# Optimization experiments

Measured on AMD Instinct MI355X. Metric: run time of the kernel, lower is better.

The kernel has to match this reference:

```python
import jax, jax.numpy as jnp
import numpy as np

N_NODES = 100000
N_EDGES = 1000000
D_IN = 64
D_OUT = 64


def setup_inputs() -> dict:
    key = jax.random.key(0)
    k_x, k_e, k_w, k_b = jax.random.split(key, 4)
    x = jax.random.normal(k_x, (N_NODES, D_IN), dtype=jnp.float32)
    edge_index = jax.random.randint(k_e, (2, N_EDGES), 0, N_NODES, dtype=jnp.int64)
    # degrees of destination nodes (what the caller is expected to supply);
    # clamp to >=1 to avoid division by zero for isolated nodes
    deg = jax.ops.segment_sum(jnp.ones((N_EDGES,), jnp.float32), edge_index[1], num_segments=N_NODES)
    node_degrees = jnp.maximum(deg, 1.0)
    W = jax.random.normal(k_w, (D_OUT, D_IN), dtype=jnp.float32) * (1.0 / np.sqrt(D_IN))
    b = jax.random.normal(k_b, (D_OUT,), dtype=jnp.float32) * 0.01
    return {"x": x, "edge_index": edge_index, "node_degrees": node_degrees, "W": W, "b": b}


def reference(x, edge_index, node_degrees, W, b):
    # Original does argsort+cumsum+boundary segment-sum; mathematically this is
    # a scatter-add of gathered neighbor features into dst, i.e. a segment sum.
    src, dst = edge_index[0], edge_index[1]
    agg = jax.ops.segment_sum(x[src], dst, num_segments=x.shape[0])  # [N, D_IN]
    mean = agg / node_degrees[:, None]
    return mean @ W.T + b  # [N, D_OUT]
```

## Files before the change

### kernel.cpp

```cpp
#include <hip/hip_runtime.h>


#define D 64
#define BSHIFT 7
#define BNODES (1 << BSHIFT)
#define CAP 2048
#define GTHREADS 512
#define PERTHREAD (CAP / GTHREADS)
#define PXW_THREADS 512
#define MAXB 2048

__device__ inline int detect_stride_block(const unsigned* __restrict__ words,
                                          int E, int* sflag) {
    int t = threadIdx.x;
    if (t < 64) {
        unsigned v = (t < E) ? words[2 * t + 1] : 0u;
        int any = __any(v != 0u);
        if (t == 0) *sflag = any ? 1 : 2;
    }
    __syncthreads();
    return *sflag;
}

__device__ inline unsigned pack_bf16(float a, float b) {
    unsigned ua = __float_as_uint(a), ub = __float_as_uint(b);
    ua += 0x7fffu + ((ua >> 16) & 1u);
    ub += 0x7fffu + ((ub >> 16) & 1u);
    return (ua >> 16) | (ub & 0xffff0000u);
}

__global__ __launch_bounds__(PXW_THREADS, 4) void partition_xw_kernel(
        const unsigned* __restrict__ ewords, int* __restrict__ cursor,
        unsigned* __restrict__ pairs, uint2* __restrict__ spill,
        int* __restrict__ spillCnt,
        const float* __restrict__ x, const float* __restrict__ W,
        unsigned* __restrict__ y2, int E, int N, int nb, int pblocks) {
    __shared__ __align__(16) char smem[52240];
    int t = threadIdx.x;

    if ((int)blockIdx.x < pblocks) {
        int* lhist = (int*)smem;
        int* lbase = lhist + MAXB;
        int* sflag = lbase + MAXB;
        int s = detect_stride_block(ewords, E, sflag);
        int base = blockIdx.x * 8192;
        for (int i = t; i < nb; i += PXW_THREADS) lhist[i] = 0;
        __syncthreads();
        unsigned pv[16]; int bk[16];
        #pragma unroll
        for (int k = 0; k < 16; ++k) {
            int e = base + k * PXW_THREADS + t;
            bk[k] = -1;
            if (e < E) {
                unsigned src = ewords[(size_t)e * s];
                unsigned dst = ewords[((size_t)E + e) * s];
                bk[k] = (int)(dst >> BSHIFT);
                pv[k] = src | ((dst & (BNODES - 1)) << 17);
                atomicAdd(&lhist[bk[k]], 1);
            }
        }
        __syncthreads();
        for (int hb = t; hb < nb; hb += PXW_THREADS) {
            int cc = lhist[hb];
            if (cc) lbase[hb] = atomicAdd(&cursor[hb], cc);
            lhist[hb] = 0;
        }
        __syncthreads();
        #pragma unroll
        for (int k = 0; k < 16; ++k) {
            if (bk[k] >= 0) {
                int lpos = lbase[bk[k]] + atomicAdd(&lhist[bk[k]], 1);
                if (lpos < CAP) {
                    pairs[(size_t)bk[k] * CAP + lpos] = pv[k];
                } else {
                    int si = atomicAdd(spillCnt, 1);
                    unsigned dst = ((unsigned)bk[k] << BSHIFT) | (pv[k] >> 17);
                    spill[si] = make_uint2(pv[k] & 0x1FFFFu, dst);
                }
            }
        }
    } else {
        float* Wt = (float*)smem;
        float* xs = Wt + 64 * 68;
        for (int i = t; i < 64 * 64; i += PXW_THREADS) {
            int o = i >> 6, k = i & 63;
            Wt[k * 68 + o] = W[i];
        }
        int base = ((int)blockIdx.x - pblocks) * 128;
        int row = t >> 4, c4 = (t & 15) * 4;
        #pragma unroll
        for (int r = 0; r < 4; ++r) {
            int nl = row + r * 32;
            int n = base + nl;
            float4 v = {0.f, 0.f, 0.f, 0.f};
            if (n < N) v = *(const float4*)(x + (size_t)n * 64 + c4);
            *(float4*)&xs[nl * 68 + c4] = v;
        }
        __syncthreads();
        int o4 = (t & 15) * 4, nl4 = (t >> 4) * 4;
        float acc[4][4];
        #pragma unroll
        for (int i = 0; i < 4; ++i)
            #pragma unroll
            for (int j = 0; j < 4; ++j) acc[i][j] = 0.f;
        #pragma unroll 2
        for (int k0 = 0; k0 < 64; k0 += 4) {
            float a[4][4], wv[4][4];
            #pragma unroll
            for (int i = 0; i < 4; ++i)
                *(float4*)a[i] = *(const float4*)&xs[(nl4 + i) * 68 + k0];
            #pragma unroll
            for (int dk = 0; dk < 4; ++dk)
                *(float4*)wv[dk] = *(const float4*)&Wt[(k0 + dk) * 68 + o4];
            #pragma unroll
            for (int i = 0; i < 4; ++i)
                #pragma unroll
                for (int j = 0; j < 4; ++j)
                    acc[i][j] += a[i][0] * wv[0][j] + a[i][1] * wv[1][j]
                               + a[i][2] * wv[2][j] + a[i][3] * wv[3][j];
        }
        int n0 = base + nl4;
        #pragma unroll
        for (int i = 0; i < 4; ++i) {
            if (n0 + i < N) {
                uint2 p;
                p.x = pack_bf16(acc[i][0], acc[i][1]);
                p.y = pack_bf16(acc[i][2], acc[i][3]);
                *(uint2*)(y2 + (size_t)(n0 + i) * 32 + (o4 >> 1)) = p;
            }
        }
    }
}

__global__ __launch_bounds__(GTHREADS) void bucket_gather(
        const unsigned* __restrict__ y2, const unsigned* __restrict__ pairs,
        const int* __restrict__ cursor, const uint2* __restrict__ spill,
        const int* __restrict__ spillCnt,
        const float* __restrict__ deg, const float* __restrict__ b,
        float* __restrict__ out, int N) {
    __shared__ unsigned list[CAP];
    __shared__ int cnt[BNODES], st[BNODES], sc[BNODES];
    int t = threadIdx.x;
    int bkt = blockIdx.x, base = bkt << BSHIFT;
    int total = cursor[bkt];
    int cn = total < CAP ? total : CAP;
    int lane = t & 63, w = t >> 6;
    int g = lane >> 4, c = lane & 15;
    float4 bv = ((const float4*)b)[c];

    if (t < BNODES) cnt[t] = 0;
    __syncthreads();
    unsigned pv[PERTHREAD];
    #pragma unroll
    for (int j = 0; j < PERTHREAD; ++j) {
        int i = t + j * GTHREADS;
        pv[j] = (i < cn) ? pairs[(size_t)bkt * CAP + i] : 0xFFFFFFFFu;
        if (i < cn) atomicAdd(&cnt[pv[j] >> 17], 1);
    }
    __syncthreads();
    if (t < BNODES) sc[t] = cnt[t];
    __syncthreads();
    for (int off = 1; off < BNODES; off <<= 1) {
        int v = (t < BNODES && t >= off) ? sc[t - off] : 0;
        __syncthreads();
        if (t < BNODES) sc[t] += v;
        __syncthreads();
    }
    if (t < BNODES) { st[t] = sc[t] - cnt[t]; sc[t] = sc[t] - cnt[t]; }
    __syncthreads();
    #pragma unroll
    for (int j = 0; j < PERTHREAD; ++j) {
        if (pv[j] != 0xFFFFFFFFu) {
            int pos = atomicAdd(&sc[pv[j] >> 17], 1);
            list[pos] = pv[j] & 0x1FFFFu;
        }
    }
    __syncthreads();

    int scnt = *spillCnt;

    for (int nl0 = w * 16; nl0 < w * 16 + 16; nl0 += 4) {
        int mynode = nl0 + g;
        int n = base + mynode;
        int s0 = st[mynode], e1 = s0 + cnt[mynode];
        float ax = 0.f, ay = 0.f, az = 0.f, aw = 0.f;
        float bx = 0.f, by = 0.f, bz = 0.f, bw = 0.f;
        int i = s0;
        for (; i + 1 < e1; i += 2) {
            unsigned s0v = list[i], s1v = list[i + 1];
            uint2 u0 = *(const uint2*)(y2 + (size_t)s0v * 32 + c * 2);
            uint2 u1 = *(const uint2*)(y2 + (size_t)s1v * 32 + c * 2);
            ax += __uint_as_float(u0.x << 16);
            ay += __uint_as_float(u0.x & 0xffff0000u);
            az += __uint_as_float(u0.y << 16);
            aw += __uint_as_float(u0.y & 0xffff0000u);
            bx += __uint_as_float(u1.x << 16);
            by += __uint_as_float(u1.x & 0xffff0000u);
            bz += __uint_as_float(u1.y << 16);
            bw += __uint_as_float(u1.y & 0xffff0000u);
        }
        if (i < e1) {
            unsigned sv = list[i];
            uint2 u = *(const uint2*)(y2 + (size_t)sv * 32 + c * 2);
            ax += __uint_as_float(u.x << 16);
            ay += __uint_as_float(u.x & 0xffff0000u);
            az += __uint_as_float(u.y << 16);
            aw += __uint_as_float(u.y & 0xffff0000u);
        }
        ax += bx; ay += by; az += bz; aw += bw;
        for (int k = 0; k < scnt; ++k) {
            uint2 e = spill[k];
            if ((int)e.y == n) {
                uint2 u = *(const uint2*)(y2 + (size_t)e.x * 32 + c * 2);
                ax += __uint_as_float(u.x << 16);
                ay += __uint_as_float(u.x & 0xffff0000u);
                az += __uint_as_float(u.y << 16);
                aw += __uint_as_float(u.y & 0xffff0000u);
            }
        }
        if (n < N) {
            float invd = 1.0f / deg[n];
            float4 o4 = {ax * invd + bv.x, ay * invd + bv.y,
                         az * invd + bv.z, aw * invd + bv.w};
            *(float4*)(out + (size_t)n * 64 + c * 4) = o4;
        }
    }
}

__global__ __launch_bounds__(256) void scatter_kernel(
        const float* __restrict__ x, const unsigned* __restrict__ ewords,
        float* __restrict__ agg, int E) {
    __shared__ int sflag;
    int s = detect_stride_block(ewords, E, &sflag);
    int gid = blockIdx.x * blockDim.x + threadIdx.x;
    int e = gid >> 4, q = gid & 15;
    if (e >= E) return;
    int src = (int)ewords[(size_t)e * s];
    int dst = (int)ewords[((size_t)E + e) * s];
    const float4 v = *(const float4*)(x + (size_t)src * D + q * 4);
    float* p = agg + (size_t)dst * D + q * 4;
    unsafeAtomicAdd(p + 0, v.x);
    unsafeAtomicAdd(p + 1, v.y);
    unsafeAtomicAdd(p + 2, v.z);
    unsafeAtomicAdd(p + 3, v.w);
}

__global__ __launch_bounds__(256) void gemm_kernel(
        float* __restrict__ inout, const float* __restrict__ deg,
        const float* __restrict__ W, const float* __restrict__ b, int nNodes) {
    __shared__ float Wt[64 * 65];
    __shared__ float rows[4 * 64];
    int t = threadIdx.x;
    for (int i = t; i < 64 * 64; i += 256) {
        int o = i >> 6, k = i & 63;
        Wt[k * 65 + o] = W[i];
    }
    int base = blockIdx.x * 4;
    int nl = t >> 6, o = t & 63;
    int n = base + nl;
    if (n < nNodes) {
        float invd = 1.0f / deg[n];
        rows[nl * 64 + o] = inout[(size_t)n * 64 + o] * invd;
    }
    __syncthreads();
    if (n >= nNodes) return;
    float acc = b[o];
    #pragma unroll
    for (int k = 0; k < 64; ++k)
        acc += rows[nl * 64 + k] * Wt[k * 65 + o];
    inout[(size_t)n * 64 + o] = acc;
}

extern "C" void kernel_launch(void* const* d_in, const int* in_sizes, int n_in,
                              void* d_out, int out_size, void* d_ws, size_t ws_size,
                              hipStream_t stream) {
    const float*    x      = (const float*)d_in[0];
    const unsigned* ewords = (const unsigned*)d_in[1];
    const float*    deg    = (const float*)d_in[2];
    const float*    W      = (const float*)d_in[3];
    const float*    b      = (const float*)d_in[4];
    float*          out    = (float*)d_out;

    const int E = in_sizes[1] / 2;
    const int N = in_sizes[2];
    const int nb = (N + BNODES - 1) >> BSHIFT;

    char* ws = (char*)d_ws;
    size_t curB  = (MAXB + 16) * 4;
    size_t pairB = ((size_t)nb * CAP * 4 + 63) & ~63ull;
    size_t spB   = ((size_t)E * 8 + 63) & ~63ull;
    size_t need  = curB + pairB + spB + (size_t)N * 32 * 4;

    if (ws_size >= need && N < (1 << 17) && nb <= MAXB) {
        int*      cursor   = (int*)ws;
        int*      spillCnt = cursor + MAXB;
        unsigned* pairs    = (unsigned*)(ws + curB);
        uint2*    spill    = (uint2*)(ws + curB + pairB);
        unsigned* y2       = (unsigned*)(ws + curB + pairB + spB);

        hipMemsetAsync(cursor, 0, curB, stream);

        int pblocks  = (E + 8191) / 8192;
        int xwblocks = (N + 127) / 128;
        partition_xw_kernel<<<pblocks + xwblocks, PXW_THREADS, 0, stream>>>(
            ewords, cursor, pairs, spill, spillCnt, x, W, y2, E, N, nb, pblocks);

        bucket_gather<<<nb, GTHREADS, 0, stream>>>(
            y2, pairs, cursor, spill, spillCnt, deg, b, out, N);
    } else {
        hipMemsetAsync(d_out, 0, (size_t)out_size * sizeof(float), stream);
        long long sthreads = (long long)E * 16;
        int sblocks = (int)((sthreads + 255) / 256);
        scatter_kernel<<<sblocks, 256, 0, stream>>>(x, ewords, out, E);
        gemm_kernel<<<(N + 3) / 4, 256, 0, stream>>>(out, deg, W, b, N);
    }
}
```

Baseline: 140.8 us.

## Fuse memset, partition/XW and bucket gather into one cooperative persistent kernel

Replaces the memset plus two kernel launches with a single cooperative kernel on a fixed grid of 512 blocks. Phases are separated by grid-wide syncs, and blocks loop over virtual partition, XW and bucket work items. The XW tile shrinks from 128 to 64 nodes per block. This is meant to remove launch gaps and inter-kernel overhead, at the cost of grid-sync latency and possible load imbalance from the fixed grid. If the cooperative launch fails, it falls back to the original path.

```diff
diff --git a/kernel.cpp b/kernel.cpp
--- a/kernel.cpp
+++ b/kernel.cpp
@@ -1,4 +1,7 @@
 #include <hip/hip_runtime.h>
+#include <hip/hip_cooperative_groups.h>
+
+namespace cg = cooperative_groups;
 
 
 #define D 64
@@ -9,6 +12,7 @@
 #define PERTHREAD (CAP / GTHREADS)
 #define PXW_THREADS 512
 #define MAXB 2048
+#define COOP_GRID 512
 
 __device__ inline int detect_stride_block(const unsigned* __restrict__ words,
                                           int E, int* sflag) {
@@ -27,6 +31,210 @@
     ua += 0x7fffu + ((ua >> 16) & 1u);
     ub += 0x7fffu + ((ub >> 16) & 1u);
     return (ua >> 16) | (ub & 0xffff0000u);
+}
+
+__global__ __launch_bounds__(512, 4) void fused_all(
+        const unsigned* __restrict__ ewords, int* __restrict__ cursor,
+        unsigned* __restrict__ pairs, uint2* __restrict__ spill,
+        int* __restrict__ spillCnt,
+        const float* __restrict__ x, const float* __restrict__ W,
+        unsigned* __restrict__ y2,
+        const float* __restrict__ deg, const float* __restrict__ bias,
+        float* __restrict__ out,
+        int E, int N, int nb, int pblocks, int xwblocks) {
+    __shared__ __align__(16) char smem[34832];
+    int t = threadIdx.x;
+    cg::grid_group grid = cg::this_grid();
+
+    for (int i = blockIdx.x * 512 + t; i < MAXB + 16; i += gridDim.x * 512)
+        cursor[i] = 0;
+    grid.sync();
+
+    for (int vb = blockIdx.x; vb < pblocks + xwblocks; vb += gridDim.x) {
+        __syncthreads();
+        if (vb < pblocks) {
+            int* lhist = (int*)smem;
+            int* lbase = lhist + MAXB;
+            int* sflag = lbase + MAXB;
+            int s = detect_stride_block(ewords, E, sflag);
+            int base = vb * 8192;
+            for (int i = t; i < nb; i += 512) lhist[i] = 0;
+            __syncthreads();
+            unsigned pv[16]; int bk[16];
+            #pragma unroll
+            for (int k = 0; k < 16; ++k) {
+                int e = base + k * 512 + t;
+                bk[k] = -1;
+                if (e < E) {
+                    unsigned src = ewords[(size_t)e * s];
+                    unsigned dst = ewords[((size_t)E + e) * s];
+                    bk[k] = (int)(dst >> BSHIFT);
+                    pv[k] = src | ((dst & (BNODES - 1)) << 17);
+                    atomicAdd(&lhist[bk[k]], 1);
+                }
+            }
+            __syncthreads();
+            for (int hb = t; hb < nb; hb += 512) {
+                int cc = lhist[hb];
+                if (cc) lbase[hb] = atomicAdd(&cursor[hb], cc);
+                lhist[hb] = 0;
+            }
+            __syncthreads();
+            #pragma unroll
+            for (int k = 0; k < 16; ++k) {
+                if (bk[k] >= 0) {
+                    int lpos = lbase[bk[k]] + atomicAdd(&lhist[bk[k]], 1);
+                    if (lpos < CAP) {
+                        pairs[(size_t)bk[k] * CAP + lpos] = pv[k];
+                    } else {
+                        int si = atomicAdd(spillCnt, 1);
+                        unsigned dst = ((unsigned)bk[k] << BSHIFT) | (pv[k] >> 17);
+                        spill[si] = make_uint2(pv[k] & 0x1FFFFu, dst);
+                    }
+                }
+            }
+        } else {
+            float* Wt = (float*)smem;
+            float* xs = Wt + 64 * 68;
+            for (int i = t; i < 64 * 64; i += 512) {
+                int o = i >> 6, k = i & 63;
+                Wt[k * 68 + o] = W[i];
+            }
+            int base = (vb - pblocks) * 64;
+            int idx = t;
+            #pragma unroll
+            for (int r = 0; r < 2; ++r, idx += 512) {
+                int nl = idx >> 4, c4 = (idx & 15) * 4;
+                int n = base + nl;
+                float4 v = {0.f, 0.f, 0.f, 0.f};
+                if (n < N) v = *(const float4*)(x + (size_t)n * 64 + c4);
+                *(float4*)&xs[nl * 68 + c4] = v;
+            }
+            __syncthreads();
+            int o4 = (t & 15) * 4, nl2 = (t >> 4) * 2;
+            float acc[2][4];
+            #pragma unroll
+            for (int i = 0; i < 2; ++i)
+                #pragma unroll
+                for (int j = 0; j < 4; ++j) acc[i][j] = 0.f;
+            #pragma unroll 2
+            for (int k0 = 0; k0 < 64; k0 += 4) {
+                float a[2][4], wv[4][4];
+                #pragma unroll
+                for (int i = 0; i < 2; ++i)
+                    *(float4*)a[i] = *(const float4*)&xs[(nl2 + i) * 68 + k0];
+                #pragma unroll
+                for (int dk = 0; dk < 4; ++dk)
+                    *(float4*)wv[dk] = *(const float4*)&Wt[(k0 + dk) * 68 + o4];
+                #pragma unroll
+                for (int i = 0; i < 2; ++i)
+                    #pragma unroll
+                    for (int j = 0; j < 4; ++j)
+                        acc[i][j] += a[i][0] * wv[0][j] + a[i][1] * wv[1][j]
+                                   + a[i][2] * wv[2][j] + a[i][3] * wv[3][j];
+            }
+            int n0 = base + nl2;
+            #pragma unroll
+            for (int i = 0; i < 2; ++i) {
+                if (n0 + i < N) {
+                    uint2 p;
+                    p.x = pack_bf16(acc[i][0], acc[i][1]);
+                    p.y = pack_bf16(acc[i][2], acc[i][3]);
+                    *(uint2*)(y2 + (size_t)(n0 + i) * 32 + (o4 >> 1)) = p;
+                }
+            }
+        }
+    }
+    grid.sync();
+
+    int lane = t & 63, w = t >> 6;
+    int g = lane >> 4, c = lane & 15;
+    float4 bv = ((const float4*)bias)[c];
+    unsigned* list = (unsigned*)smem;
+    int* cnt = (int*)(smem + 8192);
+    int* st  = cnt + BNODES;
+    int* sc  = st + BNODES;
+    for (int bkt = blockIdx.x; bkt < nb; bkt += gridDim.x) {
+        __syncthreads();
+        int base = bkt << BSHIFT;
+        int total = cursor[bkt];
+        int cn = total < CAP ? total : CAP;
+        if (t < BNODES) cnt[t] = 0;
+        __syncthreads();
+        unsigned pv[PERTHREAD];
+        #pragma unroll
+        for (int j = 0; j < PERTHREAD; ++j) {
+            int i = t + j * GTHREADS;
+            pv[j] = (i < cn) ? pairs[(size_t)bkt * CAP + i] : 0xFFFFFFFFu;
+            if (i < cn) atomicAdd(&cnt[pv[j] >> 17], 1);
+        }
+        __syncthreads();
+        if (t < BNODES) sc[t] = cnt[t];
+        __syncthreads();
+        for (int off = 1; off < BNODES; off <<= 1) {
+            int v = (t < BNODES && t >= off) ? sc[t - off] : 0;
+            __syncthreads();
+            if (t < BNODES) sc[t] += v;
+            __syncthreads();
+        }
+        if (t < BNODES) { st[t] = sc[t] - cnt[t]; sc[t] = sc[t] - cnt[t]; }
+        __syncthreads();
+        #pragma unroll
+        for (int j = 0; j < PERTHREAD; ++j) {
+            if (pv[j] != 0xFFFFFFFFu) {
+                int pos = atomicAdd(&sc[pv[j] >> 17], 1);
+                list[pos] = pv[j] & 0x1FFFFu;
+            }
+        }
+        __syncthreads();
+        int scnt = *spillCnt;
+        for (int nl0 = w * 16; nl0 < w * 16 + 16; nl0 += 4) {
+            int mynode = nl0 + g;
+            int n = base + mynode;
+            int s0 = st[mynode], e1 = s0 + cnt[mynode];
+            float ax = 0.f, ay = 0.f, az = 0.f, aw = 0.f;
+            float bx = 0.f, by = 0.f, bz = 0.f, bw = 0.f;
+            int i = s0;
+            for (; i + 1 < e1; i += 2) {
+                unsigned s0v = list[i], s1v = list[i + 1];
+                uint2 u0 = *(const uint2*)(y2 + (size_t)s0v * 32 + c * 2);
+                uint2 u1 = *(const uint2*)(y2 + (size_t)s1v * 32 + c * 2);
+                ax += __uint_as_float(u0.x << 16);
+                ay += __uint_as_float(u0.x & 0xffff0000u);
+                az += __uint_as_float(u0.y << 16);
+                aw += __uint_as_float(u0.y & 0xffff0000u);
+                bx += __uint_as_float(u1.x << 16);
+                by += __uint_as_float(u1.x & 0xffff0000u);
+                bz += __uint_as_float(u1.y << 16);
+                bw += __uint_as_float(u1.y & 0xffff0000u);
+            }
+            if (i < e1) {
+                unsigned sv = list[i];
+                uint2 u = *(const uint2*)(y2 + (size_t)sv * 32 + c * 2);
+                ax += __uint_as_float(u.x << 16);
+                ay += __uint_as_float(u.x & 0xffff0000u);
+                az += __uint_as_float(u.y << 16);
+                aw += __uint_as_float(u.y & 0xffff0000u);
+            }
+            ax += bx; ay += by; az += bz; aw += bw;
+            for (int k = 0; k < scnt; ++k) {
+                uint2 e = spill[k];
+                if ((int)e.y == n) {
+                    uint2 u = *(const uint2*)(y2 + (size_t)e.x * 32 + c * 2);
+                    ax += __uint_as_float(u.x << 16);
+                    ay += __uint_as_float(u.x & 0xffff0000u);
+                    az += __uint_as_float(u.y << 16);
+                    aw += __uint_as_float(u.y & 0xffff0000u);
+                }
+            }
+            if (n < N) {
+                float invd = 1.0f / deg[n];
+                float4 o4 = {ax * invd + bv.x, ay * invd + bv.y,
+                             az * invd + bv.z, aw * invd + bv.w};
+                *(float4*)(out + (size_t)n * 64 + c * 4) = o4;
+            }
+        }
+    }
 }
 
 __global__ __launch_bounds__(PXW_THREADS, 4) void partition_xw_kernel(
@@ -37,7 +245,6 @@
         unsigned* __restrict__ y2, int E, int N, int nb, int pblocks) {
     __shared__ __align__(16) char smem[52240];
     int t = threadIdx.x;
-
     if ((int)blockIdx.x < pblocks) {
         int* lhist = (int*)smem;
         int* lbase = lhist + MAXB;
@@ -176,9 +383,7 @@
         }
     }
     __syncthreads();
-
     int scnt = *spillCnt;
-
     for (int nl0 = w * 16; nl0 < w * 16 + 16; nl0 += 4) {
         int mynode = nl0 + g;
         int n = base + mynode;
@@ -298,15 +503,26 @@
         uint2*    spill    = (uint2*)(ws + curB + pairB);
         unsigned* y2       = (unsigned*)(ws + curB + pairB + spB);
 
-        hipMemsetAsync(cursor, 0, curB, stream);
-
-        int pblocks  = (E + 8191) / 8192;
-        int xwblocks = (N + 127) / 128;
-        partition_xw_kernel<<<pblocks + xwblocks, PXW_THREADS, 0, stream>>>(
-            ewords, cursor, pairs, spill, spillCnt, x, W, y2, E, N, nb, pblocks);
-
-        bucket_gather<<<nb, GTHREADS, 0, stream>>>(
-            y2, pairs, cursor, spill, spillCnt, deg, b, out, N);
+        int pblocks   = (E + 8191) / 8192;
+        int xw64      = (N + 63) / 64;
+
+        void* args[] = {
+            (void*)&ewords, (void*)&cursor, (void*)&pairs, (void*)&spill,
+            (void*)&spillCnt, (void*)&x, (void*)&W, (void*)&y2,
+            (void*)&deg, (void*)&b, (void*)&out,
+            (void*)&E, (void*)&N, (void*)&nb, (void*)&pblocks, (void*)&xw64
+        };
+        hipError_t err = hipLaunchCooperativeKernel(
+            (const void*)fused_all, dim3(COOP_GRID), dim3(512), args, 0, stream);
+
+        if (err != hipSuccess) {
+            hipMemsetAsync(cursor, 0, curB, stream);
+            int xwblocks = (N + 127) / 128;
+            partition_xw_kernel<<<pblocks + xwblocks, PXW_THREADS, 0, stream>>>(
+                ewords, cursor, pairs, spill, spillCnt, x, W, y2, E, N, nb, pblocks);
+            bucket_gather<<<nb, GTHREADS, 0, stream>>>(
+                y2, pairs, cursor, spill, spillCnt, deg, b, out, N);
+        }
     } else {
         hipMemsetAsync(d_out, 0, (size_t)out_size * sizeof(float), stream);
         long long sthreads = (long long)E * 16;
```

Measured after the change: 259.3 us. 1.84x slower.
